# Performance work log

Measured on AMD Instinct MI355X. Metric: run time of the kernel, lower is better.

Reference implementation:

```python
import jax, jax.numpy as jnp
import numpy as np

N_NODES = 100000
N_EDGES = 3200000
D = 256


def setup_inputs() -> dict:
    key = jax.random.key(0)
    ks = jax.random.split(key, 8)
    ego_embeddings = jax.random.normal(ks[0], (N_NODES, D), dtype=jnp.float32) * 0.1
    edge_vals = jax.random.uniform(ks[1], (N_EDGES,), dtype=jnp.float32) / 32.0  # ~normalized adjacency
    W1 = jax.random.normal(ks[2], (D, D), dtype=jnp.float32) * (1.0 / np.sqrt(D))
    b1 = jnp.zeros((D,), dtype=jnp.float32)
    W2 = jax.random.normal(ks[3], (D, D), dtype=jnp.float32) * (1.0 / np.sqrt(D))
    b2 = jnp.zeros((D,), dtype=jnp.float32)
    edge_rows = jax.random.randint(ks[4], (N_EDGES,), 0, N_NODES, dtype=jnp.int32)
    edge_cols = jax.random.randint(ks[5], (N_EDGES,), 0, N_NODES, dtype=jnp.int32)
    return {"ego_embeddings": ego_embeddings, "edge_vals": edge_vals,
            "W1": W1, "b1": b1, "W2": W2, "b2": b2,
            "edge_rows": edge_rows, "edge_cols": edge_cols}


def reference(ego_embeddings, edge_vals, W1, b1, W2, b2, edge_rows, edge_cols):
    # SpMM: side = A_in @ ego  (A_in in COO: rows, cols, vals)
    n = ego_embeddings.shape[0]
    gathered = ego_embeddings[edge_cols] * edge_vals[:, None]      # [E, D]
    side = jax.ops.segment_sum(gathered, edge_rows, num_segments=n)  # [N, D]
    # bi-interaction aggregator
    sum_emb = jax.nn.leaky_relu((ego_embeddings + side) @ W1.T + b1, negative_slope=0.01)
    bi_emb = jax.nn.leaky_relu((ego_embeddings * side) @ W2.T + b2, negative_slope=0.01)
    # dropout p=0.0 -> identity
    return sum_emb + bi_emb
```

## Files before the change

### kernel.cpp

```cpp
#include <hip/hip_runtime.h>
#include <hip/hip_fp16.h>
#include <stdint.h>

#define D 256
#define CHSH 13
#define NPW 25

typedef __attribute__((ext_vector_type(8))) short short8;
typedef __attribute__((ext_vector_type(4))) float floatx4;

__device__ __forceinline__ ushort f2bf(float f) {
    union { float f; uint32_t u; } v; v.f = f;
    uint32_t u = v.u;
    u += 0x7fffu + ((u >> 16) & 1u);
    return (ushort)(u >> 16);
}
__device__ __forceinline__ float bf2f(ushort h) {
    union { uint32_t u; float f; } v; v.u = ((uint32_t)h) << 16;
    return v.f;
}


__global__ void k_hist(const int* __restrict__ er, const int* __restrict__ ec,
                       const float* __restrict__ ev,
                       int* __restrict__ bp, uint64_t* __restrict__ aux,
                       int E, int NCH) {
    int e = blockIdx.x * 256 + threadIdx.x;
    if (e >= E) return;
    int row = er[e];
    int col = ec[e];
    int b = row * NCH + (col >> CHSH);
    atomicAdd(&bp[b], 1);
    ushort hb = __half_as_ushort(__float2half_rn(ev[e]));
    uint32_t payload = ((uint32_t)col << 15) | (uint32_t)hb;
    aux[e] = ((uint64_t)(uint32_t)b << 32) | payload;
}

__global__ void k_red(const int* __restrict__ bp, int* __restrict__ part, int nb) {
    __shared__ int s[256];
    int t = threadIdx.x;
    int base = blockIdx.x * 1024 + t * 4;
    int v = 0;
#pragma unroll
    for (int j = 0; j < 4; ++j) if (base + j < nb) v += bp[base + j];
    s[t] = v; __syncthreads();
    for (int off = 128; off; off >>= 1) {
        if (t < off) s[t] += s[t + off];
        __syncthreads();
    }
    if (t == 0) part[blockIdx.x] = s[0];
}

__global__ __launch_bounds__(1024) void k_scanpart(int* __restrict__ part, int np) {
    __shared__ int s[1024];
    int t = threadIdx.x;
    int p0 = (2 * t < np) ? part[2 * t] : 0;
    int p1 = (2 * t + 1 < np) ? part[2 * t + 1] : 0;
    int v = p0 + p1;
    s[t] = v; __syncthreads();
    for (int off = 1; off < 1024; off <<= 1) {
        int x = (t >= off) ? s[t - off] : 0;
        __syncthreads();
        s[t] += x;
        __syncthreads();
    }
    int excl = s[t] - v;
    if (2 * t < np) part[2 * t] = excl;
    if (2 * t + 1 < np) part[2 * t + 1] = excl + p0;
}

__global__ void k_scan3(int* __restrict__ bp, const int* __restrict__ part, int nb) {
    __shared__ int s[256];
    int t = threadIdx.x;
    int base = blockIdx.x * 1024 + t * 4;
    int d0 = 0, d1 = 0, d2 = 0, d3 = 0;
    if (base     < nb) d0 = bp[base];
    if (base + 1 < nb) d1 = bp[base + 1];
    if (base + 2 < nb) d2 = bp[base + 2];
    if (base + 3 < nb) d3 = bp[base + 3];
    int sum = d0 + d1 + d2 + d3;
    s[t] = sum; __syncthreads();
    for (int off = 1; off < 256; off <<= 1) {
        int x = (t >= off) ? s[t - off] : 0;
        __syncthreads();
        s[t] += x;
        __syncthreads();
    }
    int run = part[blockIdx.x] + s[t] - sum;
    if (base     < nb) bp[base]     = run; run += d0;
    if (base + 1 < nb) bp[base + 1] = run; run += d1;
    if (base + 2 < nb) bp[base + 2] = run; run += d2;
    if (base + 3 < nb) bp[base + 3] = run;
}

__global__ void k_scatter(const uint64_t* __restrict__ aux,
                          int* __restrict__ bp, uint32_t* __restrict__ csr,
                          int E, int BW) {
    int xcd = blockIdx.x & 7;
    int j = blockIdx.x >> 3;
    int e = j * 256 + threadIdx.x;
    if (e >= E) return;
    uint64_t a = aux[e];
    int b = (int)(a >> 32);
    int lo = xcd * BW;
    if (b < lo || b >= lo + BW) return;
    int p = atomicAdd(&bp[b], 1);
    csr[p] = (uint32_t)a;
}

__global__ void k_cvt(const float4* __restrict__ ego, ushort4* __restrict__ ego_bf,
                      const float4* __restrict__ W1, const float4* __restrict__ W2,
                      ushort4* __restrict__ W1b, ushort4* __restrict__ W2b, int n4) {
    int i = blockIdx.x * 256 + threadIdx.x;
    const float4* src;
    ushort4* dst;
    if (i < n4) { src = ego + i; dst = ego_bf + i; }
    else {
        int j = i - n4;
        if (j >= 32768) return;
        int k = j & 16383;
        src = ((j < 16384) ? W1 : W2) + k;
        dst = ((j < 16384) ? W1b : W2b) + k;
    }
    float4 f = *src;
    ushort4 u;
    u.x = f2bf(f.x); u.y = f2bf(f.y); u.z = f2bf(f.z); u.w = f2bf(f.w);
    *dst = u;
}

__global__ __launch_bounds__(256, 4) void k_spmm(
        const ushort* __restrict__ ego_bf, const int* __restrict__ bp,
        const uint32_t* __restrict__ csr,
        ushort* __restrict__ X1, ushort* __restrict__ X2, int n, int NCH) {
    int wid = __builtin_amdgcn_readfirstlane(blockIdx.x * 4 + (threadIdx.x >> 6));
    int lane = threadIdx.x & 63;
    int node0 = wid * NPW;
    if (node0 >= n) return;
    int d0 = lane * 4;

    float acc[NPW][4];
#pragma unroll
    for (int i = 0; i < NPW; ++i) {
        acc[i][0] = 0.f; acc[i][1] = 0.f; acc[i][2] = 0.f; acc[i][3] = 0.f;
    }

    for (int c = 0; c < NCH; ++c) {
#pragma unroll
        for (int i = 0; i < NPW; ++i) {
            int node = node0 + i;
            if (node < n) {
                int idx = node * NCH + c;
                int beg = (idx == 0) ? 0 : bp[idx - 1];
                int end = bp[idx];
                int e = beg;
                for (; e + 2 <= end; e += 2) {
                    uint32_t w0 = csr[e], w1 = csr[e + 1];
                    ushort4 u0 = *(const ushort4*)(ego_bf + (size_t)(w0 >> 15) * D + d0);
                    ushort4 u1 = *(const ushort4*)(ego_bf + (size_t)(w1 >> 15) * D + d0);
                    float v0 = __half2float(__ushort_as_half((ushort)(w0 & 0x7fff)));
                    float v1 = __half2float(__ushort_as_half((ushort)(w1 & 0x7fff)));
                    acc[i][0] += v0 * bf2f(u0.x); acc[i][1] += v0 * bf2f(u0.y);
                    acc[i][2] += v0 * bf2f(u0.z); acc[i][3] += v0 * bf2f(u0.w);
                    acc[i][0] += v1 * bf2f(u1.x); acc[i][1] += v1 * bf2f(u1.y);
                    acc[i][2] += v1 * bf2f(u1.z); acc[i][3] += v1 * bf2f(u1.w);
                }
                if (e < end) {
                    uint32_t w = csr[e];
                    float v = __half2float(__ushort_as_half((ushort)(w & 0x7fff)));
                    ushort4 u = *(const ushort4*)(ego_bf + (size_t)(w >> 15) * D + d0);
                    acc[i][0] += v * bf2f(u.x); acc[i][1] += v * bf2f(u.y);
                    acc[i][2] += v * bf2f(u.z); acc[i][3] += v * bf2f(u.w);
                }
            }
        }
    }

#pragma unroll
    for (int i = 0; i < NPW; ++i) {
        int node = node0 + i;
        if (node < n) {
            ushort4 eg = *(const ushort4*)(ego_bf + (size_t)node * D + d0);
            float e0 = bf2f(eg.x), e1 = bf2f(eg.y), e2 = bf2f(eg.z), e3 = bf2f(eg.w);
            ushort4 o1, o2;
            o1.x = f2bf(e0 + acc[i][0]); o2.x = f2bf(e0 * acc[i][0]);
            o1.y = f2bf(e1 + acc[i][1]); o2.y = f2bf(e1 * acc[i][1]);
            o1.z = f2bf(e2 + acc[i][2]); o2.z = f2bf(e2 * acc[i][2]);
            o1.w = f2bf(e3 + acc[i][3]); o2.w = f2bf(e3 * acc[i][3]);
            *(ushort4*)(X1 + (size_t)node * D + d0) = o1;
            *(ushort4*)(X2 + (size_t)node * D + d0) = o2;
        }
    }
}

__global__ __launch_bounds__(256) void k_gemm(
        const ushort* __restrict__ X1, const ushort* __restrict__ X2,
        const ushort* __restrict__ W1b, const ushort* __restrict__ W2b,
        const float* __restrict__ b1, const float* __restrict__ b2,
        float* __restrict__ out, int n) {
    int lane = threadIdx.x & 63;
    int w = threadIdx.x >> 6;
    int l16 = lane & 15, quad = lane >> 4;
    int row0 = blockIdx.x * 64;
    int colw = w * 64;

    floatx4 acc1[4][4], acc2[4][4];
#pragma unroll
    for (int i = 0; i < 4; ++i)
#pragma unroll
        for (int j = 0; j < 4; ++j) { acc1[i][j] = (floatx4)0.f; acc2[i][j] = (floatx4)0.f; }

    for (int kk = 0; kk < D; kk += 32) {
        short8 a[4], b[4];
#pragma unroll
        for (int mt = 0; mt < 4; ++mt)
            a[mt] = *(const short8*)(X1 + (size_t)(row0 + mt * 16 + l16) * D + kk + quad * 8);
#pragma unroll
        for (int nt = 0; nt < 4; ++nt)
            b[nt] = *(const short8*)(W1b + (size_t)(colw + nt * 16 + l16) * D + kk + quad * 8);
#pragma unroll
        for (int mt = 0; mt < 4; ++mt)
#pragma unroll
            for (int nt = 0; nt < 4; ++nt)
                acc1[mt][nt] = __builtin_amdgcn_mfma_f32_16x16x32_bf16(a[mt], b[nt], acc1[mt][nt], 0, 0, 0);
    }
    for (int kk = 0; kk < D; kk += 32) {
        short8 a[4], b[4];
#pragma unroll
        for (int mt = 0; mt < 4; ++mt)
            a[mt] = *(const short8*)(X2 + (size_t)(row0 + mt * 16 + l16) * D + kk + quad * 8);
#pragma unroll
        for (int nt = 0; nt < 4; ++nt)
            b[nt] = *(const short8*)(W2b + (size_t)(colw + nt * 16 + l16) * D + kk + quad * 8);
#pragma unroll
        for (int mt = 0; mt < 4; ++mt)
#pragma unroll
            for (int nt = 0; nt < 4; ++nt)
                acc2[mt][nt] = __builtin_amdgcn_mfma_f32_16x16x32_bf16(a[mt], b[nt], acc2[mt][nt], 0, 0, 0);
    }

#pragma unroll
    for (int nt = 0; nt < 4; ++nt) {
        int col = colw + nt * 16 + l16;
        float bb1 = b1[col], bb2 = b2[col];
#pragma unroll
        for (int mt = 0; mt < 4; ++mt) {
            int row = row0 + mt * 16 + quad * 4;
#pragma unroll
            for (int r = 0; r < 4; ++r) {
                if (row + r < n) {
                    float v1 = acc1[mt][nt][r] + bb1;
                    v1 = v1 > 0.f ? v1 : 0.01f * v1;
                    float v2 = acc2[mt][nt][r] + bb2;
                    v2 = v2 > 0.f ? v2 : 0.01f * v2;
                    out[(size_t)(row + r) * D + col] = v1 + v2;
                }
            }
        }
    }
}

extern "C" void kernel_launch(void* const* d_in, const int* in_sizes, int n_in,
                              void* d_out, int out_size, void* d_ws, size_t ws_size,
                              hipStream_t stream) {
    const float* ego   = (const float*)d_in[0];
    const float* evals = (const float*)d_in[1];
    const float* W1    = (const float*)d_in[2];
    const float* b1    = (const float*)d_in[3];
    const float* W2    = (const float*)d_in[4];
    const float* b2    = (const float*)d_in[5];
    const int* erows   = (const int*)d_in[6];
    const int* ecols   = (const int*)d_in[7];
    float* out = (float*)d_out;

    int n = in_sizes[0] / D;
    int E = in_sizes[1];
    int npad = (n + 63) & ~63;
    int NCH = (n + (1 << CHSH) - 1) >> CHSH;
    int nb = n * NCH;
    int np = (nb + 1023) / 1024;
    int BW = (nb + 7) / 8;

    char* p = (char*)d_ws;
    auto alloc = [&](size_t bytes) {
        char* q = p;
        p += (bytes + 511) & ~(size_t)511;
        return q;
    };
    ushort* ego_bf = (ushort*)alloc((size_t)n * D * 2);
    ushort* X1     = (ushort*)alloc((size_t)npad * D * 2);
    ushort* X2     = (ushort*)alloc((size_t)npad * D * 2);
    ushort* W1b    = (ushort*)alloc((size_t)D * D * 2);
    ushort* W2b    = (ushort*)alloc((size_t)D * D * 2);
    int* bp        = (int*)alloc((size_t)nb * 4);
    int* part      = (int*)alloc((size_t)np * 4);
    uint32_t* csr  = (uint32_t*)alloc((size_t)E * 4);

    uint64_t* aux = (uint64_t*)X1;

    hipMemsetAsync(bp, 0, (size_t)nb * 4, stream);
    int EB = (E + 255) / 256;
    k_hist<<<EB, 256, 0, stream>>>(erows, ecols, evals, bp, aux, E, NCH);
    k_red<<<np, 256, 0, stream>>>(bp, part, nb);
    k_scanpart<<<1, 1024, 0, stream>>>(part, np);
    k_scan3<<<np, 256, 0, stream>>>(bp, part, nb);
    k_scatter<<<8 * EB, 256, 0, stream>>>(aux, bp, csr, E, BW);

    int n4 = n * (D / 4);
    k_cvt<<<(n4 + 32768 + 255) / 256, 256, 0, stream>>>((const float4*)ego, (ushort4*)ego_bf,
                                                        (const float4*)W1, (const float4*)W2,
                                                        (ushort4*)W1b, (ushort4*)W2b, n4);

    int nwaves = (n + NPW - 1) / NPW;
    int nblocks = (nwaves + 3) / 4;
    k_spmm<<<nblocks, 256, 0, stream>>>(ego_bf, bp, csr, X1, X2, n, NCH);

    k_gemm<<<npad / 64, 256, 0, stream>>>(X1, X2, W1b, W2b, b1, b2, out, n);
}
```

Before: 965.7 us.

## Pad CSR buckets to multiples of four, go chunk-major, unroll SpMM by four

Bucket indices become chunk-major (chunk*n + row) instead of row-major. Each bucket's edge count is rounded up to a multiple of four, and the CSR array is zero-filled so padded slots add zero. The SpMM kernel preloads the NPW+1 bucket boundaries once per chunk and runs a four-wide unrolled loop with no remainder, which gives more independent gathers in flight. In exchange it needs a separate boundary array, a memset of a larger CSR buffer, and it reads extra padded entries, all of which point at node 0.

```diff
diff --git a/kernel.cpp b/kernel.cpp
--- a/kernel.cpp
+++ b/kernel.cpp
@@ -24,12 +24,12 @@
 __global__ void k_hist(const int* __restrict__ er, const int* __restrict__ ec,
                        const float* __restrict__ ev,
                        int* __restrict__ bp, uint64_t* __restrict__ aux,
-                       int E, int NCH) {
+                       int E, int n) {
     int e = blockIdx.x * 256 + threadIdx.x;
     if (e >= E) return;
     int row = er[e];
     int col = ec[e];
-    int b = row * NCH + (col >> CHSH);
+    int b = (col >> CHSH) * n + row;
     atomicAdd(&bp[b], 1);
     ushort hb = __half_as_ushort(__float2half_rn(ev[e]));
     uint32_t payload = ((uint32_t)col << 15) | (uint32_t)hb;
@@ -42,7 +42,7 @@
     int base = blockIdx.x * 1024 + t * 4;
     int v = 0;
 #pragma unroll
-    for (int j = 0; j < 4; ++j) if (base + j < nb) v += bp[base + j];
+    for (int j = 0; j < 4; ++j) if (base + j < nb) v += (bp[base + j] + 3) & ~3;
     s[t] = v; __syncthreads();
     for (int off = 128; off; off >>= 1) {
         if (t < off) s[t] += s[t + off];
@@ -69,16 +69,17 @@
     if (2 * t + 1 < np) part[2 * t + 1] = excl + p0;
 }
 
-__global__ void k_scan3(int* __restrict__ bp, const int* __restrict__ part, int nb) {
+__global__ void k_scan3(int* __restrict__ bp, int* __restrict__ bp2,
+                        const int* __restrict__ part, int nb) {
     __shared__ int s[256];
     int t = threadIdx.x;
     int base = blockIdx.x * 1024 + t * 4;
-    int d0 = 0, d1 = 0, d2 = 0, d3 = 0;
-    if (base     < nb) d0 = bp[base];
-    if (base + 1 < nb) d1 = bp[base + 1];
-    if (base + 2 < nb) d2 = bp[base + 2];
-    if (base + 3 < nb) d3 = bp[base + 3];
-    int sum = d0 + d1 + d2 + d3;
+    int p0 = 0, p1 = 0, p2 = 0, p3 = 0;
+    if (base     < nb) p0 = (bp[base]     + 3) & ~3;
+    if (base + 1 < nb) p1 = (bp[base + 1] + 3) & ~3;
+    if (base + 2 < nb) p2 = (bp[base + 2] + 3) & ~3;
+    if (base + 3 < nb) p3 = (bp[base + 3] + 3) & ~3;
+    int sum = p0 + p1 + p2 + p3;
     s[t] = sum; __syncthreads();
     for (int off = 1; off < 256; off <<= 1) {
         int x = (t >= off) ? s[t - off] : 0;
@@ -87,10 +88,10 @@
         __syncthreads();
     }
     int run = part[blockIdx.x] + s[t] - sum;
-    if (base     < nb) bp[base]     = run; run += d0;
-    if (base + 1 < nb) bp[base + 1] = run; run += d1;
-    if (base + 2 < nb) bp[base + 2] = run; run += d2;
-    if (base + 3 < nb) bp[base + 3] = run;
+    if (base     < nb) { bp[base]     = run; bp2[base]     = run; if (base     == nb - 1) bp2[nb] = run + p0; } run += p0;
+    if (base + 1 < nb) { bp[base + 1] = run; bp2[base + 1] = run; if (base + 1 == nb - 1) bp2[nb] = run + p1; } run += p1;
+    if (base + 2 < nb) { bp[base + 2] = run; bp2[base + 2] = run; if (base + 2 == nb - 1) bp2[nb] = run + p2; } run += p2;
+    if (base + 3 < nb) { bp[base + 3] = run; bp2[base + 3] = run; if (base + 3 == nb - 1) bp2[nb] = run + p3; }
 }
 
 __global__ void k_scatter(const uint64_t* __restrict__ aux,
@@ -129,9 +130,9 @@
 }
 
 __global__ __launch_bounds__(256, 4) void k_spmm(
-        const ushort* __restrict__ ego_bf, const int* __restrict__ bp,
+        const ushort* __restrict__ ego_bf, const int* __restrict__ bp2,
         const uint32_t* __restrict__ csr,
-        ushort* __restrict__ X1, ushort* __restrict__ X2, int n, int NCH) {
+        ushort* __restrict__ X1, ushort* __restrict__ X2, int n, int NCH, int nb) {
     int wid = __builtin_amdgcn_readfirstlane(blockIdx.x * 4 + (threadIdx.x >> 6));
     int lane = threadIdx.x & 63;
     int node0 = wid * NPW;
@@ -145,31 +146,34 @@
     }
 
     for (int c = 0; c < NCH; ++c) {
+        int B[NPW + 1];
+#pragma unroll
+        for (int i = 0; i <= NPW; ++i) {
+            int idx = c * n + node0 + i;
+            B[i] = bp2[idx > nb ? nb : idx];
+        }
 #pragma unroll
         for (int i = 0; i < NPW; ++i) {
-            int node = node0 + i;
-            if (node < n) {
-                int idx = node * NCH + c;
-                int beg = (idx == 0) ? 0 : bp[idx - 1];
-                int end = bp[idx];
-                int e = beg;
-                for (; e + 2 <= end; e += 2) {
-                    uint32_t w0 = csr[e], w1 = csr[e + 1];
+            if (node0 + i < n) {
+                int end = B[i + 1];
+                for (int e = B[i]; e < end; e += 4) {
+                    uint32_t w0 = csr[e], w1 = csr[e + 1], w2 = csr[e + 2], w3 = csr[e + 3];
                     ushort4 u0 = *(const ushort4*)(ego_bf + (size_t)(w0 >> 15) * D + d0);
                     ushort4 u1 = *(const ushort4*)(ego_bf + (size_t)(w1 >> 15) * D + d0);
+                    ushort4 u2 = *(const ushort4*)(ego_bf + (size_t)(w2 >> 15) * D + d0);
+                    ushort4 u3 = *(const ushort4*)(ego_bf + (size_t)(w3 >> 15) * D + d0);
                     float v0 = __half2float(__ushort_as_half((ushort)(w0 & 0x7fff)));
                     float v1 = __half2float(__ushort_as_half((ushort)(w1 & 0x7fff)));
+                    float v2 = __half2float(__ushort_as_half((ushort)(w2 & 0x7fff)));
+                    float v3 = __half2float(__ushort_as_half((ushort)(w3 & 0x7fff)));
                     acc[i][0] += v0 * bf2f(u0.x); acc[i][1] += v0 * bf2f(u0.y);
                     acc[i][2] += v0 * bf2f(u0.z); acc[i][3] += v0 * bf2f(u0.w);
                     acc[i][0] += v1 * bf2f(u1.x); acc[i][1] += v1 * bf2f(u1.y);
                     acc[i][2] += v1 * bf2f(u1.z); acc[i][3] += v1 * bf2f(u1.w);
-                }
-                if (e < end) {
-                    uint32_t w = csr[e];
-                    float v = __half2float(__ushort_as_half((ushort)(w & 0x7fff)));
-                    ushort4 u = *(const ushort4*)(ego_bf + (size_t)(w >> 15) * D + d0);
-                    acc[i][0] += v * bf2f(u.x); acc[i][1] += v * bf2f(u.y);
-                    acc[i][2] += v * bf2f(u.z); acc[i][3] += v * bf2f(u.w);
+                    acc[i][0] += v2 * bf2f(u2.x); acc[i][1] += v2 * bf2f(u2.y);
+                    acc[i][2] += v2 * bf2f(u2.z); acc[i][3] += v2 * bf2f(u2.w);
+                    acc[i][0] += v3 * bf2f(u3.x); acc[i][1] += v3 * bf2f(u3.y);
+                    acc[i][2] += v3 * bf2f(u3.z); acc[i][3] += v3 * bf2f(u3.w);
                 }
             }
         }
@@ -279,6 +283,7 @@
     int nb = n * NCH;
     int np = (nb + 1023) / 1024;
     int BW = (nb + 7) / 8;
+    size_t csr_cap = (size_t)E + 3u * (size_t)nb;
 
     char* p = (char*)d_ws;
     auto alloc = [&](size_t bytes) {
@@ -292,17 +297,19 @@
     ushort* W1b    = (ushort*)alloc((size_t)D * D * 2);
     ushort* W2b    = (ushort*)alloc((size_t)D * D * 2);
     int* bp        = (int*)alloc((size_t)nb * 4);
+    int* bp2       = (int*)alloc((size_t)(nb + 64) * 4);
     int* part      = (int*)alloc((size_t)np * 4);
-    uint32_t* csr  = (uint32_t*)alloc((size_t)E * 4);
+    uint32_t* csr  = (uint32_t*)alloc(csr_cap * 4);
 
     uint64_t* aux = (uint64_t*)X1;
 
     hipMemsetAsync(bp, 0, (size_t)nb * 4, stream);
+    hipMemsetAsync(csr, 0, csr_cap * 4, stream);
     int EB = (E + 255) / 256;
-    k_hist<<<EB, 256, 0, stream>>>(erows, ecols, evals, bp, aux, E, NCH);
+    k_hist<<<EB, 256, 0, stream>>>(erows, ecols, evals, bp, aux, E, n);
     k_red<<<np, 256, 0, stream>>>(bp, part, nb);
     k_scanpart<<<1, 1024, 0, stream>>>(part, np);
-    k_scan3<<<np, 256, 0, stream>>>(bp, part, nb);
+    k_scan3<<<np, 256, 0, stream>>>(bp, bp2, part, nb);
     k_scatter<<<8 * EB, 256, 0, stream>>>(aux, bp, csr, E, BW);
 
     int n4 = n * (D / 4);
@@ -312,7 +319,7 @@
 
     int nwaves = (n + NPW - 1) / NPW;
     int nblocks = (nwaves + 3) / 4;
-    k_spmm<<<nblocks, 256, 0, stream>>>(ego_bf, bp, csr, X1, X2, n, NCH);
+    k_spmm<<<nblocks, 256, 0, stream>>>(ego_bf, bp2, csr, X1, X2, n, NCH, nb);
 
     k_gemm<<<npad / 64, 256, 0, stream>>>(X1, X2, W1b, W2b, b1, b2, out, n);
 }
```

Measured after the change: 867.6 us. -10.2%, faster.
